# Optimization experiments

Measured on AMD Instinct MI355X. Metric: run time of the kernel, lower is better.

## Reference

```python
import jax, jax.numpy as jnp
import numpy as np

N = 100_000   # nodes
D = 64        # hidden = H * C
H, C = 8, 8   # heads, per-head channels
E = 500_000   # edges per edge set
EPS = 1e-3    # keras LayerNormalization default epsilon
RSQRT_C = np.float32(1.0 / np.sqrt(C))


def setup_inputs() -> dict:
    key = jax.random.key(0)
    ks = jax.random.split(key, 13)
    s = 0.05
    return dict(
        x=jax.random.normal(ks[0], (N, D), jnp.float32),
        src0=jax.random.randint(ks[1], (E,), 0, N, jnp.int32),
        dst0=jax.random.randint(ks[2], (E,), 0, N, jnp.int32),
        src1=jax.random.randint(ks[3], (E,), 0, N, jnp.int32),
        dst1=jax.random.randint(ks[4], (E,), 0, N, jnp.int32),
        Wk=jax.random.normal(ks[5], (D, D), jnp.float32) * s,
        bk=jnp.zeros((D,), jnp.float32),
        Wm=jax.random.normal(ks[6], (D, D), jnp.float32) * s,
        bm=jnp.zeros((D,), jnp.float32),
        Wq=jax.random.normal(ks[7], (D, D), jnp.float32) * s,
        bq=jnp.zeros((D,), jnp.float32),
        Wa=jax.random.normal(ks[8], (D, D), jnp.float32) * s,
        ba=jnp.zeros((D,), jnp.float32),
        Watt0=jax.random.normal(ks[9], (H, C, C), jnp.float32) * s,
        Wmsg0=jax.random.normal(ks[10], (H, C, C), jnp.float32) * s,
        prior0=jnp.ones((H,), jnp.float32),
        Watt1=jax.random.normal(ks[11], (H, C, C), jnp.float32) * s,
        Wmsg1=jax.random.normal(ks[12], (H, C, C), jnp.float32) * s,
        prior1=jnp.ones((H,), jnp.float32),
        skip_w=jnp.ones((1,), jnp.float32),
        ln_gamma=jnp.ones((D,), jnp.float32),
        ln_beta=jnp.zeros((D,), jnp.float32),
    )


def _edge_terms(k, m, q, src, dst, Watt, Wmsg, prior):
    # gather sender keys/messages, apply per-edge-set per-head projections
    ke = jnp.einsum('ehk,hkl->ehl', k[src], Watt)          # [E,H,C]
    score = jnp.einsum('ehc,ehc->eh', ke, q[dst]) * prior * RSQRT_C  # [E,H]
    me = jnp.einsum('ehk,hkl->ehl', m[src], Wmsg)          # [E,H,C]
    return score, me


def _forward(x, src0, dst0, src1, dst1, Wk, bk, Wm, bm, Wq, bq, Wa, ba,
             Watt0, Wmsg0, prior0, Watt1, Wmsg1, prior1,
             skip_w, ln_gamma, ln_beta):
    n = x.shape[0]
    split = lambda t: t.reshape(n, H, C)
    k = split(x @ Wk + bk)   # sender keys   [N,H,C]
    m = split(x @ Wm + bm)   # sender msgs   [N,H,C]
    q = split(x @ Wq + bq)   # receiver qrys [N,H,C]

    s0, m0 = _edge_terms(k, m, q, src0, dst0, Watt0, Wmsg0, prior0)
    s1, m1 = _edge_terms(k, m, q, src1, dst1, Watt1, Wmsg1, prior1)

    # joint segment softmax over ALL incoming edges per receiver (across edge sets)
    scores = jnp.concatenate([s0, s1], axis=0)  # [Et,H]
    msgs = jnp.concatenate([m0, m1], axis=0)    # [Et,H,C]
    recv = jnp.concatenate([dst0, dst1], axis=0)
    smax = jax.ops.segment_max(scores, recv, num_segments=n)
    ex = jnp.exp(scores - smax[recv])
    denom = jax.ops.segment_sum(ex, recv, num_segments=n)
    coef = ex / denom[recv]                      # [Et,H]

    pooled = jax.ops.segment_sum(coef[:, :, None] * msgs, recv, num_segments=n)  # [N,H,C]
    merged = pooled.reshape(n, D)
    agg = jax.nn.gelu(merged, approximate=False) @ Wa + ba
    # (dropout_rate=0.0 -> identity)
    sc = jax.nn.sigmoid(skip_w[0])               # learnable weighted skip
    out = sc * agg + (1.0 - sc) * x
    # layer norm (keras default eps=1e-3)
    mu = jnp.mean(out, axis=-1, keepdims=True)
    var = jnp.var(out, axis=-1, keepdims=True)
    return ln_gamma * (out - mu) * jax.lax.rsqrt(var + EPS) + ln_beta


def reference(x, src0, dst0, src1, dst1, Wk, bk, Wm, bm, Wq, bq, Wa, ba,
              Watt0, Wmsg0, prior0, Watt1, Wmsg1, prior1,
              skip_w, ln_gamma, ln_beta):
    return _forward(x, src0, dst0, src1, dst1, Wk, bk, Wm, bm, Wq, bq, Wa, ba,
                    Watt0, Wmsg0, prior0, Watt1, Wmsg1, prior1,
                    skip_w, ln_gamma, ln_beta)
```

## Files before the change

kernel.cpp:

```cpp
#include <hip/hip_runtime.h>
#include <cstdint>
#include <cstddef>

#define TPB 256
static constexpr float RSQRT_C_F = 0.35355339059327373f;

typedef __attribute__((ext_vector_type(8))) short bf16x8;
typedef __attribute__((ext_vector_type(4))) float f32x4;

__device__ __forceinline__ unsigned short f2bf(float f) {
    unsigned u = __float_as_uint(f);
    u += 0x7FFFu + ((u >> 16) & 1u);
    return (unsigned short)(u >> 16);
}
__device__ __forceinline__ float bf2f(unsigned short h) {
    return __uint_as_float((unsigned)h << 16);
}
__device__ __forceinline__ float loF(unsigned u) { return __uint_as_float(u << 16); }
__device__ __forceinline__ float hiF(unsigned u) { return __uint_as_float(u); }

__global__ void prep1_kernel(const float* __restrict__ Wq, const float* __restrict__ bq,
                             const float* __restrict__ Wk, const float* __restrict__ bk,
                             const float* __restrict__ Wm, const float* __restrict__ bm,
                             const float* __restrict__ Watt0, const float* __restrict__ prior0,
                             const float* __restrict__ Watt1, const float* __restrict__ prior1,
                             const float* __restrict__ Wmsg0, const float* __restrict__ Wmsg1,
                             float* __restrict__ Wbig, float* __restrict__ bbig) {
    int idx = blockIdx.x * TPB + threadIdx.x;
    if (idx < 64 * 320) {
        int i = idx / 320, col = idx % 320;
        float v;
        if (col < 64) {
            v = Wq[i * 64 + col];
        } else {
            int j = col - 64, set = j >> 6, l = j & 63, h = l >> 3, lc = l & 7;
            const float* Win = (set < 2) ? Wk : Wm;
            const float* T = (set == 0) ? Watt0 : (set == 1) ? Watt1 : (set == 2) ? Wmsg0 : Wmsg1;
            float scale = (set == 0) ? prior0[h] * RSQRT_C_F
                        : (set == 1) ? prior1[h] * RSQRT_C_F : 1.f;
            float acc = 0.f;
            #pragma unroll
            for (int c = 0; c < 8; c++) acc += Win[i * 64 + h * 8 + c] * T[h * 64 + c * 8 + lc];
            v = acc * scale;
        }
        Wbig[idx] = v;
    } else if (idx < 64 * 320 + 320) {
        int col = idx - 64 * 320;
        float v;
        if (col < 64) {
            v = bq[col];
        } else {
            int j = col - 64, set = j >> 6, l = j & 63, h = l >> 3, lc = l & 7;
            const float* bin = (set < 2) ? bk : bm;
            const float* T = (set == 0) ? Watt0 : (set == 1) ? Watt1 : (set == 2) ? Wmsg0 : Wmsg1;
            float scale = (set == 0) ? prior0[h] * RSQRT_C_F
                        : (set == 1) ? prior1[h] * RSQRT_C_F : 1.f;
            float acc = 0.f;
            #pragma unroll
            for (int c = 0; c < 8; c++) acc += bin[h * 8 + c] * T[h * 64 + c * 8 + lc];
            v = acc * scale;
        }
        bbig[col] = v;
    }
}

__global__ void prep2_kernel(const float* __restrict__ Wbig, const float* __restrict__ Wa,
                             unsigned short* __restrict__ Wpack,
                             unsigned short* __restrict__ Wapack) {
    int p = blockIdx.x * TPB + threadIdx.x;
    bool isWa = (p >= 40 * 64);
    if (p >= 48 * 64) return;
    int pl = isWa ? p - 40 * 64 : p;
    int lane = pl & 63, ctkt = pl >> 6;
    int ct = ctkt >> 1, kt = ctkt & 1;
    int kbase = kt * 32 + (lane >> 4) * 8;
    int col = ct * 16 + (lane & 15);
    const float* W = isWa ? Wa : Wbig;
    const int stride = isWa ? 64 : 320;
    unsigned short h[8];
    #pragma unroll
    for (int j = 0; j < 8; j++) h[j] = f2bf(W[(size_t)(kbase + j) * stride + col]);
    uint4 pk;
    pk.x = (unsigned)h[0] | ((unsigned)h[1] << 16);
    pk.y = (unsigned)h[2] | ((unsigned)h[3] << 16);
    pk.z = (unsigned)h[4] | ((unsigned)h[5] << 16);
    pk.w = (unsigned)h[6] | ((unsigned)h[7] << 16);
    unsigned short* dst = isWa ? Wapack : Wpack;
    *(uint4*)&dst[(size_t)pl * 8] = pk;
}

__global__ void hist_kernel(const int* __restrict__ dst0, const int* __restrict__ dst1,
                            int* __restrict__ sub, int* __restrict__ rank,
                            int E0, int Etot, int N) {
    int e = blockIdx.x * TPB + threadIdx.x;
    if (e >= Etot) return;
    int d = (e < E0) ? dst0[e] : dst1[e - E0];
    d = min(max(d, 0), N - 1);
    int s = blockIdx.x & 7;
    rank[e] = atomicAdd(&sub[s * N + d], 1);
}

__global__ void sumsub_kernel(int* __restrict__ sub, int* __restrict__ count, int N) {
    int d = blockIdx.x * TPB + threadIdx.x;
    if (d >= N) return;
    int s = 0;
    #pragma unroll
    for (int b = 0; b < 8; b++) {
        int t = sub[b * N + d];
        sub[b * N + d] = s;
        s += t;
    }
    count[d] = s;
}

__global__ void scan1(const int* __restrict__ count, int* __restrict__ offsets,
                      int* __restrict__ blocksums, int n) {
    __shared__ int sums[TPB];
    int b = blockIdx.x, t = threadIdx.x;
    int base = b * 1024 + t * 4;
    int c0 = (base + 0 < n) ? count[base + 0] : 0;
    int c1 = (base + 1 < n) ? count[base + 1] : 0;
    int c2 = (base + 2 < n) ? count[base + 2] : 0;
    int c3 = (base + 3 < n) ? count[base + 3] : 0;
    int local = c0 + c1 + c2 + c3;
    sums[t] = local;
    __syncthreads();
    for (int off = 1; off < TPB; off <<= 1) {
        int add = (t >= off) ? sums[t - off] : 0;
        __syncthreads();
        sums[t] += add;
        __syncthreads();
    }
    int excl = sums[t] - local;
    if (base + 0 < n) offsets[base + 0] = excl;
    if (base + 1 < n) offsets[base + 1] = excl + c0;
    if (base + 2 < n) offsets[base + 2] = excl + c0 + c1;
    if (base + 3 < n) offsets[base + 3] = excl + c0 + c1 + c2;
    if (t == TPB - 1) blocksums[b] = sums[TPB - 1];
}

__global__ void scan2(int* __restrict__ blocksums, int nb) {
    __shared__ int s[TPB];
    int t = threadIdx.x;
    int v = (t < nb) ? blocksums[t] : 0;
    s[t] = v;
    __syncthreads();
    for (int off = 1; off < TPB; off <<= 1) {
        int add = (t >= off) ? s[t - off] : 0;
        __syncthreads();
        s[t] += add;
        __syncthreads();
    }
    if (t < nb) blocksums[t] = s[t] - v;
}

__global__ void scan3(int* __restrict__ offsets, const int* __restrict__ blocksums,
                      int* __restrict__ sub, int n, int Etot) {
    int i = blockIdx.x * TPB + threadIdx.x;
    if (i < n) {
        int v = offsets[i] + blocksums[i >> 10];
        offsets[i] = v;
        #pragma unroll
        for (int b = 0; b < 8; b++) sub[b * n + i] += v;
    }
    if (i == n) offsets[n] = Etot;
}

__global__ void scatter_kernel(const int* __restrict__ src0, const int* __restrict__ dst0,
                               const int* __restrict__ src1, const int* __restrict__ dst1,
                               const int* __restrict__ sub,
                               const int* __restrict__ rank, unsigned* __restrict__ records,
                               int E0, int Etot, int N) {
    int e = blockIdx.x * TPB + threadIdx.x;
    if (e >= Etot) return;
    int s, d, setbit;
    if (e < E0) { s = src0[e]; d = dst0[e]; setbit = 0; }
    else        { s = src1[e - E0]; d = dst1[e - E0]; setbit = 1; }
    d = min(max(d, 0), N - 1);
    int sb = (e >> 8) & 7;
    int pos = sub[sb * N + d] + rank[e];
    pos = min(max(pos, 0), Etot - 1);
    records[pos] = (unsigned)s | ((unsigned)setbit << 24);
}

__global__ __launch_bounds__(TPB) void proj_mfma(const float* __restrict__ x,
                                                 const unsigned short* __restrict__ Wpack,
                                                 const float* __restrict__ bbig,
                                                 unsigned short* __restrict__ qbuf,
                                                 unsigned short* __restrict__ kmbuf,
                                                 int N) {
    const int lane = threadIdx.x & 63;
    const int wv = threadIdx.x >> 6;
    const int rowbase = blockIdx.x * 64 + wv * 16;
    const int arow = min(rowbase + (lane & 15), N - 1);
    const int kbase = (lane >> 4) * 8;

    bf16x8 afrag[2];
    #pragma unroll
    for (int kt = 0; kt < 2; kt++) {
        const float* xp = x + (size_t)arow * 64 + kt * 32 + kbase;
        float4 v0 = *(const float4*)xp;
        float4 v1 = *(const float4*)(xp + 4);
        bf16x8 a;
        a[0] = (short)f2bf(v0.x); a[1] = (short)f2bf(v0.y);
        a[2] = (short)f2bf(v0.z); a[3] = (short)f2bf(v0.w);
        a[4] = (short)f2bf(v1.x); a[5] = (short)f2bf(v1.y);
        a[6] = (short)f2bf(v1.z); a[7] = (short)f2bf(v1.w);
        afrag[kt] = a;
    }

    const int colq = lane & 15;
    const int rgrp = (lane >> 4) * 4;

    for (int ct = 0; ct < 20; ct++) {
        bf16x8 b0 = *(const bf16x8*)(Wpack + ((size_t)(ct * 2 + 0) * 64 + lane) * 8);
        bf16x8 b1 = *(const bf16x8*)(Wpack + ((size_t)(ct * 2 + 1) * 64 + lane) * 8);
        f32x4 acc = {0.f, 0.f, 0.f, 0.f};
        acc = __builtin_amdgcn_mfma_f32_16x16x32_bf16(afrag[0], b0, acc, 0, 0, 0);
        acc = __builtin_amdgcn_mfma_f32_16x16x32_bf16(afrag[1], b1, acc, 0, 0, 0);
        const int col = ct * 16 + colq;
        const float bv = bbig[col];
        if (ct < 4) {
            #pragma unroll
            for (int r = 0; r < 4; r++) {
                int row = rowbase + rgrp + r;
                if (row < N) qbuf[(size_t)row * 64 + col] = f2bf(acc[r] + bv);
            }
        } else {
            const int kmcol = col - 64;
            #pragma unroll
            for (int r = 0; r < 4; r++) {
                int row = rowbase + rgrp + r;
                if (row < N) kmbuf[(size_t)row * 256 + kmcol] = f2bf(acc[r] + bv);
            }
        }
    }
}

__global__ __launch_bounds__(TPB) void pool_kernel(const unsigned short* __restrict__ qbuf,
                                                   const unsigned short* __restrict__ kmbuf,
                                                   const unsigned* __restrict__ records,
                                                   const int* __restrict__ offsets,
                                                   unsigned short* __restrict__ pooledN,
                                                   int N) {
    const int lane = threadIdx.x & 63;
    const int j = lane & 7;
    const int r = ((blockIdx.x * TPB + threadIdx.x) >> 6) * 8 + (lane >> 3);
    if (r >= N) return;
    const int beg = offsets[r], end = offsets[r + 1];

    uint4 qv = *(const uint4*)(qbuf + (size_t)r * 64 + (j << 3));
    float qa0 = loF(qv.x), qa1 = hiF(qv.x), qa2 = loF(qv.y), qa3 = hiF(qv.y);
    float qa4 = loF(qv.z), qa5 = hiF(qv.z), qa6 = loF(qv.w), qa7 = hiF(qv.w);

    float d_run = 0.f;
    float p0 = 0.f, p1 = 0.f, p2 = 0.f, p3 = 0.f, p4 = 0.f, p5 = 0.f, p6 = 0.f, p7 = 0.f;

#define EDGE(T) {                                                              \
        unsigned rec = records[T];                                             \
        size_t base = ((size_t)(rec & 0xFFFFFFu) << 8) + (((rec >> 24) & 1u) << 6) + (j << 3); \
        uint4 kv = *(const uint4*)(kmbuf + base);                              \
        uint4 mv = *(const uint4*)(kmbuf + base + 128);                        \
        float s = loF(kv.x) * qa0 + hiF(kv.x) * qa1                            \
                + loF(kv.y) * qa2 + hiF(kv.y) * qa3                            \
                + loF(kv.z) * qa4 + hiF(kv.z) * qa5                            \
                + loF(kv.w) * qa6 + hiF(kv.w) * qa7;                           \
        float c = __expf(fminf(s, 60.f));                                      \
        d_run += c;                                                            \
        p0 += c * loF(mv.x); p1 += c * hiF(mv.x);                              \
        p2 += c * loF(mv.y); p3 += c * hiF(mv.y);                              \
        p4 += c * loF(mv.z); p5 += c * hiF(mv.z);                              \
        p6 += c * loF(mv.w); p7 += c * hiF(mv.w);                              \
    }

    int t = beg;
    for (; t + 1 < end; t += 2) { EDGE(t); EDGE(t + 1); }
    if (t < end) EDGE(t);
#undef EDGE

    const float inv = (end > beg) ? 1.f / d_run : 0.f;
    uint4 ov;
    ov.x = (unsigned)f2bf(p0 * inv) | ((unsigned)f2bf(p1 * inv) << 16);
    ov.y = (unsigned)f2bf(p2 * inv) | ((unsigned)f2bf(p3 * inv) << 16);
    ov.z = (unsigned)f2bf(p4 * inv) | ((unsigned)f2bf(p5 * inv) << 16);
    ov.w = (unsigned)f2bf(p6 * inv) | ((unsigned)f2bf(p7 * inv) << 16);
    *(uint4*)(pooledN + (size_t)r * 64 + (j << 3)) = ov;
}

__global__ __launch_bounds__(TPB) void final_mfma(const float* __restrict__ x,
                                                  const unsigned short* __restrict__ pooledN,
                                                  const unsigned short* __restrict__ Wapack,
                                                  const float* __restrict__ ba,
                                                  const float* __restrict__ skipw,
                                                  const float* __restrict__ gamma,
                                                  const float* __restrict__ beta,
                                                  float* __restrict__ out, int N) {
    const int lane = threadIdx.x & 63;
    const int wv = threadIdx.x >> 6;
    const int rowbase = blockIdx.x * 64 + wv * 16;
    const int arow = min(rowbase + (lane & 15), N - 1);
    const int kbase = (lane >> 4) * 8;
    const float sc = 1.f / (1.f + __expf(-skipw[0]));

    bf16x8 afrag[2];
    #pragma unroll
    for (int kt = 0; kt < 2; kt++) {
        uint4 pv = *(const uint4*)(pooledN + (size_t)arow * 64 + kt * 32 + kbase);
        float g[8];
        g[0] = loF(pv.x); g[1] = bf2f((unsigned short)(pv.x >> 16));
        g[2] = loF(pv.y); g[3] = bf2f((unsigned short)(pv.y >> 16));
        g[4] = loF(pv.z); g[5] = bf2f((unsigned short)(pv.z >> 16));
        g[6] = loF(pv.w); g[7] = bf2f((unsigned short)(pv.w >> 16));
        bf16x8 a;
        #pragma unroll
        for (int i = 0; i < 8; i++) {
            float gg = 0.5f * g[i] * (1.f + erff(g[i] * 0.70710678118654752f));
            a[i] = (short)f2bf(gg);
        }
        afrag[kt] = a;
    }

    const int colq = lane & 15;
    const int rgrp = (lane >> 4) * 4;

    float o[4][4];
    #pragma unroll
    for (int ct = 0; ct < 4; ct++) {
        bf16x8 b0 = *(const bf16x8*)(Wapack + ((size_t)(ct * 2 + 0) * 64 + lane) * 8);
        bf16x8 b1 = *(const bf16x8*)(Wapack + ((size_t)(ct * 2 + 1) * 64 + lane) * 8);
        f32x4 acc = {0.f, 0.f, 0.f, 0.f};
        acc = __builtin_amdgcn_mfma_f32_16x16x32_bf16(afrag[0], b0, acc, 0, 0, 0);
        acc = __builtin_amdgcn_mfma_f32_16x16x32_bf16(afrag[1], b1, acc, 0, 0, 0);
        const int col = ct * 16 + colq;
        const float bav = ba[col];
        #pragma unroll
        for (int r = 0; r < 4; r++) {
            int row = min(rowbase + rgrp + r, N - 1);
            float xv = x[(size_t)row * 64 + col];
            o[ct][r] = sc * (acc[r] + bav) + (1.f - sc) * xv;
        }
    }

    #pragma unroll
    for (int r = 0; r < 4; r++) {
        float s1 = o[0][r] + o[1][r] + o[2][r] + o[3][r];
        float s2 = o[0][r] * o[0][r] + o[1][r] * o[1][r]
                 + o[2][r] * o[2][r] + o[3][r] * o[3][r];
        #pragma unroll
        for (int off = 1; off <= 8; off <<= 1) {
            s1 += __shfl_xor(s1, off, 64);
            s2 += __shfl_xor(s2, off, 64);
        }
        float mu = s1 * (1.f / 64.f);
        float var = s2 * (1.f / 64.f) - mu * mu;
        float rs = rsqrtf(var + 1e-3f);
        const int row = rowbase + rgrp + r;
        if (row < N) {
            #pragma unroll
            for (int ct = 0; ct < 4; ct++) {
                const int col = ct * 16 + colq;
                out[(size_t)row * 64 + col] = gamma[col] * (o[ct][r] - mu) * rs + beta[col];
            }
        }
    }
}

extern "C" void kernel_launch(void* const* d_in, const int* in_sizes, int n_in,
                              void* d_out, int out_size, void* d_ws, size_t ws_size,
                              hipStream_t stream) {
    const float* x      = (const float*)d_in[0];
    const int*   src0   = (const int*)d_in[1];
    const int*   dst0   = (const int*)d_in[2];
    const int*   src1   = (const int*)d_in[3];
    const int*   dst1   = (const int*)d_in[4];
    const float* Wk     = (const float*)d_in[5];
    const float* bk     = (const float*)d_in[6];
    const float* Wm     = (const float*)d_in[7];
    const float* bm     = (const float*)d_in[8];
    const float* Wq     = (const float*)d_in[9];
    const float* bq     = (const float*)d_in[10];
    const float* Wa     = (const float*)d_in[11];
    const float* ba     = (const float*)d_in[12];
    const float* Watt0  = (const float*)d_in[13];
    const float* Wmsg0  = (const float*)d_in[14];
    const float* prior0 = (const float*)d_in[15];
    const float* Watt1  = (const float*)d_in[16];
    const float* Wmsg1  = (const float*)d_in[17];
    const float* prior1 = (const float*)d_in[18];
    const float* skipw  = (const float*)d_in[19];
    const float* gamma  = (const float*)d_in[20];
    const float* beta   = (const float*)d_in[21];

    const int N  = in_sizes[0] / 64;
    const int E0 = in_sizes[1];
    const int E1 = in_sizes[3];
    const int Etot = E0 + E1;

    float* ws       = (float*)d_ws;
    float* Wbig     = ws;
    float* bbig     = Wbig + 64 * 320;
    unsigned short* Wpack  = (unsigned short*)(bbig + 320);
    unsigned short* Wapack = Wpack + 40 * 64 * 8;
    unsigned short* qbuf   = Wapack + 8 * 64 * 8;
    unsigned short* pooledN = qbuf + (size_t)N * 64;
    unsigned short* kmbuf  = pooledN + (size_t)N * 64;
    int* sub        = (int*)(kmbuf + (size_t)N * 256);
    int* count      = sub + (size_t)8 * N;
    int* offsets    = count + N;
    int* blocksums  = offsets + N + 1;
    int* rank       = blocksums + 512;
    unsigned* records = (unsigned*)(rank + Etot);

    const int nb1 = (N + 1023) / 1024;
    const int gE = (Etot + TPB - 1) / TPB;

    prep1_kernel<<<(64 * 320 + 320 + TPB - 1) / TPB, TPB, 0, stream>>>(
        Wq, bq, Wk, bk, Wm, bm, Watt0, prior0, Watt1, prior1, Wmsg0, Wmsg1, Wbig, bbig);
    hipMemsetAsync(sub, 0, (size_t)8 * N * sizeof(int), stream);
    prep2_kernel<<<(48 * 64 + TPB - 1) / TPB, TPB, 0, stream>>>(Wbig, Wa, Wpack, Wapack);

    proj_mfma<<<(N + 63) / 64, TPB, 0, stream>>>(x, Wpack, bbig, qbuf, kmbuf, N);

    hist_kernel<<<gE, TPB, 0, stream>>>(dst0, dst1, sub, rank, E0, Etot, N);
    sumsub_kernel<<<(N + TPB - 1) / TPB, TPB, 0, stream>>>(sub, count, N);

    scan1<<<nb1, TPB, 0, stream>>>(count, offsets, blocksums, N);
    scan2<<<1, TPB, 0, stream>>>(blocksums, nb1);
    scan3<<<(N + 1 + TPB - 1) / TPB, TPB, 0, stream>>>(offsets, blocksums, sub, N, Etot);

    scatter_kernel<<<gE, TPB, 0, stream>>>(src0, dst0, src1, dst1, sub,
                                           rank, records, E0, Etot, N);

    pool_kernel<<<((size_t)N * 8 + TPB - 1) / TPB, TPB, 0, stream>>>(qbuf, kmbuf, records,
                                                                     offsets, pooledN, N);

    final_mfma<<<(N + 63) / 64, TPB, 0, stream>>>(x, pooledN, Wapack, ba, skipw,
                                                  gamma, beta, (float*)d_out, N);
}
```

Before: 163.0 us.

## Fuse projection with histogram, fold subcount prefix into scan, interleave k/m layout

The projection GEMM and the destination histogram now run in one launch, with blocks split by index, so the two independent phases can overlap. The per-sub-bucket prefix sum is folded into scan1, which removes the sumsub kernel and the count array. The kmbuf layout is reordered so each head's key and message values sit next to each other (k then m, 16 bf16 per head per set), which lets pool_kernel read both from one contiguous 32-byte span. Costs are scattered 2-byte stores in the projection and strided loads of sub inside scan1.

```diff
diff --git a/kernel.cpp b/kernel.cpp
--- a/kernel.cpp
+++ b/kernel.cpp
@@ -89,40 +89,100 @@
     *(uint4*)&dst[(size_t)pl * 8] = pk;
 }
 
-__global__ void hist_kernel(const int* __restrict__ dst0, const int* __restrict__ dst1,
-                            int* __restrict__ sub, int* __restrict__ rank,
-                            int E0, int Etot, int N) {
-    int e = blockIdx.x * TPB + threadIdx.x;
-    if (e >= Etot) return;
-    int d = (e < E0) ? dst0[e] : dst1[e - E0];
-    d = min(max(d, 0), N - 1);
-    int s = blockIdx.x & 7;
-    rank[e] = atomicAdd(&sub[s * N + d], 1);
-}
-
-__global__ void sumsub_kernel(int* __restrict__ sub, int* __restrict__ count, int N) {
-    int d = blockIdx.x * TPB + threadIdx.x;
-    if (d >= N) return;
-    int s = 0;
-    #pragma unroll
-    for (int b = 0; b < 8; b++) {
-        int t = sub[b * N + d];
-        sub[b * N + d] = s;
-        s += t;
-    }
-    count[d] = s;
-}
-
-__global__ void scan1(const int* __restrict__ count, int* __restrict__ offsets,
+__global__ __launch_bounds__(TPB) void proj_hist(const float* __restrict__ x,
+                                                 const unsigned short* __restrict__ Wpack,
+                                                 const float* __restrict__ bbig,
+                                                 unsigned short* __restrict__ qbuf,
+                                                 unsigned short* __restrict__ kmbuf,
+                                                 int N, int projBlocks,
+                                                 const int* __restrict__ dst0,
+                                                 const int* __restrict__ dst1,
+                                                 int* __restrict__ sub,
+                                                 int* __restrict__ rank,
+                                                 int E0, int Etot) {
+    if (blockIdx.x >= (unsigned)projBlocks) {
+        int b = blockIdx.x - projBlocks;
+        int e = b * TPB + threadIdx.x;
+        if (e >= Etot) return;
+        int d = (e < E0) ? dst0[e] : dst1[e - E0];
+        d = min(max(d, 0), N - 1);
+        rank[e] = atomicAdd(&sub[(b & 7) * N + d], 1);
+        return;
+    }
+    const int lane = threadIdx.x & 63;
+    const int wv = threadIdx.x >> 6;
+    const int rowbase = blockIdx.x * 64 + wv * 16;
+    const int arow = min(rowbase + (lane & 15), N - 1);
+    const int kbase = (lane >> 4) * 8;
+
+    bf16x8 afrag[2];
+    #pragma unroll
+    for (int kt = 0; kt < 2; kt++) {
+        const float* xp = x + (size_t)arow * 64 + kt * 32 + kbase;
+        float4 v0 = *(const float4*)xp;
+        float4 v1 = *(const float4*)(xp + 4);
+        bf16x8 a;
+        a[0] = (short)f2bf(v0.x); a[1] = (short)f2bf(v0.y);
+        a[2] = (short)f2bf(v0.z); a[3] = (short)f2bf(v0.w);
+        a[4] = (short)f2bf(v1.x); a[5] = (short)f2bf(v1.y);
+        a[6] = (short)f2bf(v1.z); a[7] = (short)f2bf(v1.w);
+        afrag[kt] = a;
+    }
+
+    const int colq = lane & 15;
+    const int rgrp = (lane >> 4) * 4;
+
+    for (int ct = 0; ct < 20; ct++) {
+        bf16x8 b0 = *(const bf16x8*)(Wpack + ((size_t)(ct * 2 + 0) * 64 + lane) * 8);
+        bf16x8 b1 = *(const bf16x8*)(Wpack + ((size_t)(ct * 2 + 1) * 64 + lane) * 8);
+        f32x4 acc = {0.f, 0.f, 0.f, 0.f};
+        acc = __builtin_amdgcn_mfma_f32_16x16x32_bf16(afrag[0], b0, acc, 0, 0, 0);
+        acc = __builtin_amdgcn_mfma_f32_16x16x32_bf16(afrag[1], b1, acc, 0, 0, 0);
+        const int col = ct * 16 + colq;
+        const float bv = bbig[col];
+        if (ct < 4) {
+            #pragma unroll
+            for (int r = 0; r < 4; r++) {
+                int row = rowbase + rgrp + r;
+                if (row < N) qbuf[(size_t)row * 64 + col] = f2bf(acc[r] + bv);
+            }
+        } else {
+            const int cm = col - 64;
+            const int g = cm >> 6;
+            const int w = cm & 63;
+            const int h = w >> 3, c = w & 7;
+            const int set = g & 1, ism = g >> 1;
+            const int addr = set * 128 + h * 16 + ism * 8 + c;
+            #pragma unroll
+            for (int r = 0; r < 4; r++) {
+                int row = rowbase + rgrp + r;
+                if (row < N) kmbuf[(size_t)row * 256 + addr] = f2bf(acc[r] + bv);
+            }
+        }
+    }
+}
+
+__global__ void scan1(int* __restrict__ sub, int* __restrict__ offsets,
                       int* __restrict__ blocksums, int n) {
     __shared__ int sums[TPB];
     int b = blockIdx.x, t = threadIdx.x;
     int base = b * 1024 + t * 4;
-    int c0 = (base + 0 < n) ? count[base + 0] : 0;
-    int c1 = (base + 1 < n) ? count[base + 1] : 0;
-    int c2 = (base + 2 < n) ? count[base + 2] : 0;
-    int c3 = (base + 3 < n) ? count[base + 3] : 0;
-    int local = c0 + c1 + c2 + c3;
+    int cnt[4];
+    #pragma unroll
+    for (int i = 0; i < 4; i++) {
+        int d = base + i;
+        int s = 0;
+        if (d < n) {
+            #pragma unroll
+            for (int bb = 0; bb < 8; bb++) {
+                int v = sub[bb * n + d];
+                sub[bb * n + d] = s;
+                s += v;
+            }
+        }
+        cnt[i] = s;
+    }
+    int local = cnt[0] + cnt[1] + cnt[2] + cnt[3];
     sums[t] = local;
     __syncthreads();
     for (int off = 1; off < TPB; off <<= 1) {
@@ -133,9 +193,9 @@
     }
     int excl = sums[t] - local;
     if (base + 0 < n) offsets[base + 0] = excl;
-    if (base + 1 < n) offsets[base + 1] = excl + c0;
-    if (base + 2 < n) offsets[base + 2] = excl + c0 + c1;
-    if (base + 3 < n) offsets[base + 3] = excl + c0 + c1 + c2;
+    if (base + 1 < n) offsets[base + 1] = excl + cnt[0];
+    if (base + 2 < n) offsets[base + 2] = excl + cnt[0] + cnt[1];
+    if (base + 3 < n) offsets[base + 3] = excl + cnt[0] + cnt[1] + cnt[2];
     if (t == TPB - 1) blocksums[b] = sums[TPB - 1];
 }
 
@@ -183,60 +243,6 @@
     records[pos] = (unsigned)s | ((unsigned)setbit << 24);
 }
 
-__global__ __launch_bounds__(TPB) void proj_mfma(const float* __restrict__ x,
-                                                 const unsigned short* __restrict__ Wpack,
-                                                 const float* __restrict__ bbig,
-                                                 unsigned short* __restrict__ qbuf,
-                                                 unsigned short* __restrict__ kmbuf,
-                                                 int N) {
-    const int lane = threadIdx.x & 63;
-    const int wv = threadIdx.x >> 6;
-    const int rowbase = blockIdx.x * 64 + wv * 16;
-    const int arow = min(rowbase + (lane & 15), N - 1);
-    const int kbase = (lane >> 4) * 8;
-
-    bf16x8 afrag[2];
-    #pragma unroll
-    for (int kt = 0; kt < 2; kt++) {
-        const float* xp = x + (size_t)arow * 64 + kt * 32 + kbase;
-        float4 v0 = *(const float4*)xp;
-        float4 v1 = *(const float4*)(xp + 4);
-        bf16x8 a;
-        a[0] = (short)f2bf(v0.x); a[1] = (short)f2bf(v0.y);
-        a[2] = (short)f2bf(v0.z); a[3] = (short)f2bf(v0.w);
-        a[4] = (short)f2bf(v1.x); a[5] = (short)f2bf(v1.y);
-        a[6] = (short)f2bf(v1.z); a[7] = (short)f2bf(v1.w);
-        afrag[kt] = a;
-    }
-
-    const int colq = lane & 15;
-    const int rgrp = (lane >> 4) * 4;
-
-    for (int ct = 0; ct < 20; ct++) {
-        bf16x8 b0 = *(const bf16x8*)(Wpack + ((size_t)(ct * 2 + 0) * 64 + lane) * 8);
-        bf16x8 b1 = *(const bf16x8*)(Wpack + ((size_t)(ct * 2 + 1) * 64 + lane) * 8);
-        f32x4 acc = {0.f, 0.f, 0.f, 0.f};
-        acc = __builtin_amdgcn_mfma_f32_16x16x32_bf16(afrag[0], b0, acc, 0, 0, 0);
-        acc = __builtin_amdgcn_mfma_f32_16x16x32_bf16(afrag[1], b1, acc, 0, 0, 0);
-        const int col = ct * 16 + colq;
-        const float bv = bbig[col];
-        if (ct < 4) {
-            #pragma unroll
-            for (int r = 0; r < 4; r++) {
-                int row = rowbase + rgrp + r;
-                if (row < N) qbuf[(size_t)row * 64 + col] = f2bf(acc[r] + bv);
-            }
-        } else {
-            const int kmcol = col - 64;
-            #pragma unroll
-            for (int r = 0; r < 4; r++) {
-                int row = rowbase + rgrp + r;
-                if (row < N) kmbuf[(size_t)row * 256 + kmcol] = f2bf(acc[r] + bv);
-            }
-        }
-    }
-}
-
 __global__ __launch_bounds__(TPB) void pool_kernel(const unsigned short* __restrict__ qbuf,
                                                    const unsigned short* __restrict__ kmbuf,
                                                    const unsigned* __restrict__ records,
@@ -258,9 +264,9 @@
 
 #define EDGE(T) {                                                              \
         unsigned rec = records[T];                                             \
-        size_t base = ((size_t)(rec & 0xFFFFFFu) << 8) + (((rec >> 24) & 1u) << 6) + (j << 3); \
+        size_t base = ((size_t)(rec & 0xFFFFFFu) << 8) + (((rec >> 24) & 1u) << 7) + (j << 4); \
         uint4 kv = *(const uint4*)(kmbuf + base);                              \
-        uint4 mv = *(const uint4*)(kmbuf + base + 128);                        \
+        uint4 mv = *(const uint4*)(kmbuf + base + 8);                          \
         float s = loF(kv.x) * qa0 + hiF(kv.x) * qa1                            \
                 + loF(kv.y) * qa2 + hiF(kv.y) * qa3                            \
                 + loF(kv.z) * qa4 + hiF(kv.z) * qa5                            \
@@ -405,26 +411,25 @@
     unsigned short* pooledN = qbuf + (size_t)N * 64;
     unsigned short* kmbuf  = pooledN + (size_t)N * 64;
     int* sub        = (int*)(kmbuf + (size_t)N * 256);
-    int* count      = sub + (size_t)8 * N;
-    int* offsets    = count + N;
+    int* offsets    = sub + (size_t)8 * N;
     int* blocksums  = offsets + N + 1;
     int* rank       = blocksums + 512;
     unsigned* records = (unsigned*)(rank + Etot);
 
     const int nb1 = (N + 1023) / 1024;
     const int gE = (Etot + TPB - 1) / TPB;
+    const int projBlocks = (N + 63) / 64;
 
     prep1_kernel<<<(64 * 320 + 320 + TPB - 1) / TPB, TPB, 0, stream>>>(
         Wq, bq, Wk, bk, Wm, bm, Watt0, prior0, Watt1, prior1, Wmsg0, Wmsg1, Wbig, bbig);
     hipMemsetAsync(sub, 0, (size_t)8 * N * sizeof(int), stream);
     prep2_kernel<<<(48 * 64 + TPB - 1) / TPB, TPB, 0, stream>>>(Wbig, Wa, Wpack, Wapack);
 
-    proj_mfma<<<(N + 63) / 64, TPB, 0, stream>>>(x, Wpack, bbig, qbuf, kmbuf, N);
-
-    hist_kernel<<<gE, TPB, 0, stream>>>(dst0, dst1, sub, rank, E0, Etot, N);
-    sumsub_kernel<<<(N + TPB - 1) / TPB, TPB, 0, stream>>>(sub, count, N);
-
-    scan1<<<nb1, TPB, 0, stream>>>(count, offsets, blocksums, N);
+    proj_hist<<<projBlocks + gE, TPB, 0, stream>>>(x, Wpack, bbig, qbuf, kmbuf, N,
+                                                   projBlocks, dst0, dst1, sub, rank,
+                                                   E0, Etot);
+
+    scan1<<<nb1, TPB, 0, stream>>>(sub, offsets, blocksums, N);
     scan2<<<1, TPB, 0, stream>>>(blocksums, nb1);
     scan3<<<(N + 1 + TPB - 1) / TPB, TPB, 0, stream>>>(offsets, blocksums, sub, N, Etot);
 
```

Result: slower. 191.5 us (+17.5%).
